# Performance work log

Measured on AMD Instinct MI355X. Metric: run time of the kernel, lower is better.

Reference implementation:

```python
import jax, jax.numpy as jnp
import numpy as np

L, N, EMB, H = 4, 50000, 128, 4
R, HID, LBL = 16, 64, 32
E = 625000


def setup_inputs() -> dict:
    key = jax.random.key(0)
    ks = jax.random.split(key, 10)
    s = 0.05
    return {
        "embedding": jax.random.normal(ks[0], (L, N, EMB), jnp.float32),
        "in_proj_w": jax.random.normal(ks[1], (3 * EMB, EMB), jnp.float32) * s,
        "in_proj_b": jnp.zeros((3 * EMB,), jnp.float32),
        "out_proj_w": jax.random.normal(ks[2], (EMB, EMB), jnp.float32) * s,
        "out_proj_b": jnp.zeros((EMB,), jnp.float32),
        "w1": jax.random.normal(ks[3], (R, EMB, HID), jnp.float32) * s,
        "root1": jax.random.normal(ks[4], (EMB, HID), jnp.float32) * s,
        "b1": jnp.zeros((HID,), jnp.float32),
        "w2": jax.random.normal(ks[5], (R, HID, LBL), jnp.float32) * s,
        "root2": jax.random.normal(ks[6], (HID, LBL), jnp.float32) * s,
        "b2": jnp.zeros((LBL,), jnp.float32),
        "edge_index": jax.random.randint(ks[7], (2, E), 0, N, dtype=jnp.int64),
        "edge_type": jax.random.randint(ks[8], (E,), 0, R, dtype=jnp.int64),
    }


def mha_self(x, wi, bi, wo, bo):
    # x: (L, N, EMB) -- torch nn.MultiheadAttention, batch_first=False, q=k=v=x
    Ls, Ns, Es = x.shape
    hd = Es // H
    qkv = x @ wi.T + bi                      # (L, N, 3E)
    q, k, v = jnp.split(qkv, 3, axis=-1)
    q = q.reshape(Ls, Ns, H, hd)
    k = k.reshape(Ls, Ns, H, hd)
    v = v.reshape(Ls, Ns, H, hd)
    scores = jnp.einsum('lnhd,mnhd->nhlm', q, k) / np.sqrt(hd).astype(np.float32)
    attn = jax.nn.softmax(scores, axis=-1)
    out = jnp.einsum('nhlm,mnhd->lnhd', attn, v).reshape(Ls, Ns, Es)
    return out @ wo.T + bo


def rgcn_layer(x, src, dst, etype, W, root, bias):
    # PyG RGCNConv (num_bases=None, aggr='mean'):
    # out[n] = x[n] @ root + bias + sum_r mean_{e: dst=n, type=r} x[src_e] @ W[r]
    Rr, fin, fout = W.shape
    seg = etype * N + dst                                   # (E,) combined (rel, dst)
    msg_sum = jax.ops.segment_sum(x[src], seg, num_segments=Rr * N)   # (R*N, fin)
    cnt = jax.ops.segment_sum(jnp.ones((src.shape[0],), x.dtype), seg,
                              num_segments=Rr * N)
    mean = (msg_sum / jnp.maximum(cnt, 1.0)[:, None]).reshape(Rr, N, fin)
    agg = jnp.einsum('rni,rio->no', mean, W)                # per-relation GEMM
    return agg + x @ root + bias


def reference(embedding, in_proj_w, in_proj_b, out_proj_w, out_proj_b,
              w1, root1, b1, w2, root2, b2, edge_index, edge_type):
    attn_out = mha_self(embedding, in_proj_w, in_proj_b, out_proj_w, out_proj_b)
    x = attn_out[0]                                         # (N, EMB)
    src, dst = edge_index[0], edge_index[1]
    x = jax.nn.relu(rgcn_layer(x, src, dst, edge_type, w1, root1, b1))
    x = rgcn_layer(x, src, dst, edge_type, w2, root2, b2)
    return jax.nn.softmax(x, axis=-1)
```

## Files before the change

kernel.cpp:

```cpp
#include <hip/hip_runtime.h>
#include <hip/hip_bf16.h>
#include <math.h>

#define NNODES 50000
#define NEDGE 625000
#define RREL 16
#define SCAN_NB 196

typedef __attribute__((ext_vector_type(8))) short short8;
typedef __attribute__((ext_vector_type(4))) float f32x4;

__device__ __forceinline__ float bfu(ushort u) {
  return __uint_as_float(((unsigned)u) << 16);
}
__device__ __forceinline__ ushort f2b(float f) {
  __hip_bfloat16 h = __float2bfloat16(f);
  return *(ushort*)&h;
}

__global__ __launch_bounds__(256) void prep_weights(
    const float* __restrict__ ipw, const float* __restrict__ opw,
    const float* __restrict__ w1, const float* __restrict__ root1,
    const float* __restrict__ w2, const float* __restrict__ root2,
    __hip_bfloat16* __restrict__ BTqkv, __hip_bfloat16* __restrict__ BToutT,
    __hip_bfloat16* __restrict__ BT1, __hip_bfloat16* __restrict__ BT2) {
  int i = blockIdx.x * 256 + threadIdx.x;
  if (i < 49152) {
    BTqkv[i] = __float2bfloat16(ipw[i]);
  } else if (i < 65536) {
    int j = i - 49152; int m = j / 128, c = j % 128;
    BToutT[j] = __float2bfloat16(opw[c * 128 + m]);
  } else if (i < 65536 + 139264) {
    int j = i - 65536; int c = j / 128, k = j % 128;
    float v;
    if (c < 64) v = root1[k * 64 + c];
    else { int r = (c - 64) >> 6, o = (c - 64) & 63; v = w1[r * 8192 + k * 64 + o]; }
    BT1[j] = __float2bfloat16(v);
  } else if (i < 65536 + 139264 + 34816) {
    int j = i - 65536 - 139264; int c = j / 64, k = j % 64;
    float v;
    if (c < 32) v = root2[k * 32 + c];
    else { int r = (c - 32) >> 5, o = (c - 32) & 31; v = w2[r * 2048 + k * 32 + o]; }
    BT2[j] = __float2bfloat16(v);
  }
}

__global__ __launch_bounds__(256) void prep_bias1(
    const float* __restrict__ opb, const float* __restrict__ w1,
    const float* __restrict__ root1, float* __restrict__ bias1) {
  int j = blockIdx.x * 256 + threadIdx.x;
  if (j >= 1088) return;
  float s = 0.f;
  if (j < 64) {
    for (int c = 0; c < 128; c++) s += opb[c] * root1[c * 64 + j];
  } else {
    int r = (j - 64) >> 6, o = (j - 64) & 63;
    for (int c = 0; c < 128; c++) s += opb[c] * w1[r * 8192 + c * 64 + o];
  }
  bias1[j] = s;
}

__global__ __launch_bounds__(256) void qkv_gemm(
    const float* __restrict__ A, const __hip_bfloat16* __restrict__ BT,
    const float* __restrict__ bias, __hip_bfloat16* __restrict__ C) {
  __shared__ ushort As[128 * 128];
  __shared__ ushort Cs[128 * 136];
  const int t = threadIdx.x;
  const long row0 = (long)blockIdx.x * 128;

#pragma unroll
  for (int c = t; c < 128 * 16; c += 256) {
    int r = c >> 4, cc = c & 15;
    long gm = row0 + r;
    int4 v = make_int4(0, 0, 0, 0);
    if (gm < 200000) {
      const float* ap = A + gm * 128 + cc * 8;
      float4 f0 = *(const float4*)ap;
      float4 f1 = *(const float4*)(ap + 4);
      v.x = (int)f2b(f0.x) | ((int)f2b(f0.y) << 16);
      v.y = (int)f2b(f0.z) | ((int)f2b(f0.w) << 16);
      v.z = (int)f2b(f1.x) | ((int)f2b(f1.y) << 16);
      v.w = (int)f2b(f1.z) | ((int)f2b(f1.w) << 16);
    }
    *(int4*)(As + r * 128 + ((cc ^ (r & 7)) * 8)) = v;
  }
  __syncthreads();

  const int lane = t & 63, w = t >> 6;
  const int wr = (w >> 1) * 64, wc = (w & 1) * 64;
  const int lrow = lane & 15, lk = lane >> 4;
  const int nstrips = (row0 < NNODES) ? 3 : 2;

  for (int s = 0; s < nstrips; s++) {
    const int col0 = (s == 2) ? 0 : 128 + s * 128;
    const long Meff = (s == 2) ? NNODES : 200000;

    const ushort* bp[4];
#pragma unroll
    for (int j = 0; j < 4; j++)
      bp[j] = (const ushort*)BT + (long)(col0 + wc + j * 16 + lrow) * 128 + lk * 8;

    f32x4 acc[4][4];
#pragma unroll
    for (int i = 0; i < 4; i++)
#pragma unroll
      for (int j = 0; j < 4; j++) acc[i][j] = (f32x4){0.f, 0.f, 0.f, 0.f};

#pragma unroll
    for (int k0 = 0; k0 < 128; k0 += 32) {
      const int cb = k0 / 8 + lk;
      short8 af[4], bfr[4];
#pragma unroll
      for (int j = 0; j < 4; j++) bfr[j] = *(const short8*)(bp[j] + k0);
#pragma unroll
      for (int i = 0; i < 4; i++) {
        int ra = wr + i * 16 + lrow;
        af[i] = *(const short8*)(As + ra * 128 + ((cb ^ (ra & 7)) * 8));
      }
#pragma unroll
      for (int i = 0; i < 4; i++)
#pragma unroll
        for (int j = 0; j < 4; j++)
          acc[i][j] = __builtin_amdgcn_mfma_f32_16x16x32_bf16(af[i], bfr[j], acc[i][j], 0, 0, 0);
    }

    __syncthreads();
#pragma unroll
    for (int j = 0; j < 4; j++) {
      int coll = wc + j * 16 + lrow;
      float bv = bias[col0 + coll];
#pragma unroll
      for (int i = 0; i < 4; i++) {
        int rbase = wr + i * 16 + lk * 4;
#pragma unroll
        for (int q = 0; q < 4; q++)
          Cs[(rbase + q) * 136 + coll] = f2b(acc[i][j][q] + bv);
      }
    }
    __syncthreads();
#pragma unroll
    for (int idx = t; idx < 128 * 16; idx += 256) {
      int r = idx >> 4, k = idx & 15;
      long gm = row0 + r;
      if (gm < Meff)
        *(int4*)((ushort*)C + gm * 384 + col0 + k * 8) = *(const int4*)(Cs + r * 136 + k * 8);
    }
  }
}

#define EPILOGUE_STORE(MEFF, NCOLS, LDC, BIASEXPR)                              \
  for (int p = 0; p < 2; p++) {                                                 \
    __syncthreads();                                                            \
    if ((w >> 1) == p) {                                                        \
      _Pragma("unroll")                                                         \
      for (int j = 0; j < 4; j++) {                                             \
        int coll = wc + j * 16 + lrow;                                          \
        float bv = (BIASEXPR);                                                  \
        _Pragma("unroll")                                                       \
        for (int i = 0; i < 4; i++) {                                           \
          int rloc = i * 16 + lk * 4;                                           \
          _Pragma("unroll")                                                     \
          for (int q = 0; q < 4; q++)                                           \
            Cs[(rloc + q) * 132 + coll] = f2b(acc[i][j][q] + bv);               \
        }                                                                       \
      }                                                                         \
    }                                                                           \
    __syncthreads();                                                            \
    _Pragma("unroll")                                                           \
    for (int idx = t; idx < 64 * 16; idx += 256) {                              \
      int r = idx >> 4, k = idx & 15;                                           \
      long gm = row0 + p * 64 + r;                                              \
      int col = col0 + k * 8;                                                   \
      if (gm < (MEFF) && col < (NCOLS))                                         \
        *(int4*)((ushort*)C + gm * (LDC) + col) = *(const int4*)(Cs + r * 132 + k * 8); \
    }                                                                           \
  }

template <int K>
__global__ __launch_bounds__(256) void gemm_strips(
    const __hip_bfloat16* __restrict__ Av, const __hip_bfloat16* __restrict__ BT,
    const float* __restrict__ bias, __hip_bfloat16* __restrict__ C,
    int M, int N, int ldc, int spg) {
  constexpr int CPR = K / 8;
  __shared__ ushort As[128 * K];
  __shared__ ushort Cs[64 * 132];
  const int t = threadIdx.x;
  const long row0 = (long)blockIdx.x * 128;

#pragma unroll
  for (int c = t; c < 128 * CPR; c += 256) {
    int r = c / CPR, cc = c % CPR;
    long gm = row0 + r;
    int4 v = make_int4(0, 0, 0, 0);
    if (gm < M) v = *(const int4*)((const ushort*)Av + gm * K + cc * 8);
    *(int4*)(As + r * K + ((cc ^ (r & 7)) * 8)) = v;
  }
  __syncthreads();

  const int lane = t & 63, w = t >> 6;
  const int wr = (w >> 1) * 64, wc = (w & 1) * 64;
  const int lrow = lane & 15, lk = lane >> 4;
  const int nstrips = (N + 127) / 128;
  const int sbeg = blockIdx.y * spg;
  const int send = min(sbeg + spg, nstrips);

  for (int s = sbeg; s < send; s++) {
    const int col0 = s * 128;

    const ushort* bp[4];
#pragma unroll
    for (int j = 0; j < 4; j++) {
      int gn = col0 + wc + j * 16 + lrow;
      if (gn > N - 1) gn = N - 1;
      bp[j] = (const ushort*)BT + (long)gn * K + lk * 8;
    }

    f32x4 acc[4][4];
#pragma unroll
    for (int i = 0; i < 4; i++)
#pragma unroll
      for (int j = 0; j < 4; j++) acc[i][j] = (f32x4){0.f, 0.f, 0.f, 0.f};

#pragma unroll
    for (int k0 = 0; k0 < K; k0 += 32) {
      const int cb = k0 / 8 + lk;
      short8 af[4], bfr[4];
#pragma unroll
      for (int j = 0; j < 4; j++) bfr[j] = *(const short8*)(bp[j] + k0);
#pragma unroll
      for (int i = 0; i < 4; i++) {
        int ra = wr + i * 16 + lrow;
        af[i] = *(const short8*)(As + ra * K + ((cb ^ (ra & 7)) * 8));
      }
#pragma unroll
      for (int i = 0; i < 4; i++)
#pragma unroll
        for (int j = 0; j < 4; j++)
          acc[i][j] = __builtin_amdgcn_mfma_f32_16x16x32_bf16(af[i], bfr[j], acc[i][j], 0, 0, 0);
    }

    EPILOGUE_STORE(M, N, ldc, bias ? bias[min(col0 + coll, N - 1)] : 0.f)
  }
}

__global__ __launch_bounds__(256) void attn_kernel(
    const __hip_bfloat16* __restrict__ qkv, __hip_bfloat16* __restrict__ o0) {
  int w = threadIdx.x >> 6, lane = threadIdx.x & 63;
  int n = blockIdx.x * 4 + w;
  const ushort* base = (const ushort*)qkv;
  uint qv = *(const uint*)(base + (size_t)n * 384 + lane * 2);
  float q0 = bfu(qv & 0xffff), q1 = bfu(qv >> 16);
  float s[4];
#pragma unroll
  for (int m = 0; m < 4; m++) {
    uint kk = *(const uint*)(base + (size_t)(m * NNODES + n) * 384 + 128 + lane * 2);
    float p = q0 * bfu(kk & 0xffff) + q1 * bfu(kk >> 16);
#pragma unroll
    for (int off = 8; off; off >>= 1) p += __shfl_xor(p, off);
    s[m] = p * 0.17677669529663687f;
  }
  float mx = fmaxf(fmaxf(s[0], s[1]), fmaxf(s[2], s[3]));
  float e[4], sum = 0.f;
#pragma unroll
  for (int m = 0; m < 4; m++) { e[m] = __expf(s[m] - mx); sum += e[m]; }
  float inv = 1.0f / sum;
  float o0f = 0.f, o1f = 0.f;
#pragma unroll
  for (int m = 0; m < 4; m++) {
    uint vv = *(const uint*)(base + (size_t)(m * NNODES + n) * 384 + 256 + lane * 2);
    float wgt = e[m] * inv;
    o0f += wgt * bfu(vv & 0xffff);
    o1f += wgt * bfu(vv >> 16);
  }
  *(uint*)((ushort*)o0 + (size_t)n * 128 + lane * 2) = (uint)f2b(o0f) | ((uint)f2b(o1f) << 16);
}

__global__ __launch_bounds__(256) void count_edges(
    const int* __restrict__ dst, const int* __restrict__ et, int* __restrict__ cnt) {
  int e = blockIdx.x * 256 + threadIdx.x;
  if (e < NEDGE) atomicAdd(&cnt[et[e] * NNODES + dst[e]], 1);
}

__global__ __launch_bounds__(256) void scan1(
    const int* __restrict__ cnt, int* __restrict__ off, int* __restrict__ part) {
  int t = threadIdx.x, b = blockIdx.x;
  int i = b * 256 + t;
  int v = 0;
  if (i < NNODES) {
#pragma unroll
    for (int r = 0; r < RREL; r++) v += cnt[r * NNODES + i];
  }
  __shared__ int sm[256];
  sm[t] = v;
  __syncthreads();
#pragma unroll
  for (int o = 1; o < 256; o <<= 1) {
    int x = (t >= o) ? sm[t - o] : 0;
    __syncthreads();
    sm[t] += x;
    __syncthreads();
  }
  if (i < NNODES) off[i] = sm[t] - v;
  if (t == 255) part[b] = sm[t];
}

__global__ __launch_bounds__(256) void scan2(int* __restrict__ part) {
  int t = threadIdx.x;
  int v = (t < SCAN_NB) ? part[t] : 0;
  __shared__ int sm[256];
  sm[t] = v;
  __syncthreads();
#pragma unroll
  for (int o = 1; o < 256; o <<= 1) {
    int x = (t >= o) ? sm[t - o] : 0;
    __syncthreads();
    sm[t] += x;
    __syncthreads();
  }
  if (t < SCAN_NB) part[t] = sm[t] - v;
}

__global__ __launch_bounds__(256) void scan3(int* __restrict__ off, const int* __restrict__ part) {
  int i = blockIdx.x * 256 + threadIdx.x;
  if (i < NNODES) off[i] += part[blockIdx.x];
  if (i == 0) off[NNODES] = NEDGE;
}

__global__ __launch_bounds__(256) void scatter_edges(
    const int* __restrict__ src, const int* __restrict__ dst, const int* __restrict__ et,
    const int* __restrict__ cnt, const int* __restrict__ off,
    int* __restrict__ fill, unsigned* __restrict__ sorted, float* __restrict__ scales) {
  int e = blockIdx.x * 256 + threadIdx.x;
  if (e >= NEDGE) return;
  int d = dst[e], r = et[e], s = src[e];
  int pos = off[d] + atomicAdd(&fill[d], 1);
  sorted[pos] = (unsigned)s | ((unsigned)r << 16);
  scales[pos] = 1.0f / (float)cnt[r * NNODES + d];
}

__global__ __launch_bounds__(256) void fused1(
    const int* __restrict__ off, const unsigned* __restrict__ sorted,
    const float* __restrict__ scales, const ushort* __restrict__ Y1,
    const float* __restrict__ b1, __hip_bfloat16* __restrict__ x1b) {
  int w = threadIdx.x >> 6, lane = threadIdx.x & 63;
  int d = blockIdx.x * 4 + w;
  int s0 = off[d], s1 = off[d + 1];
  float a0 = bfu(Y1[(size_t)d * 1088 + lane]) + b1[lane];
  float a1 = 0.f, a2 = 0.f, a3 = 0.f;
  int i = s0;
  for (; i + 3 < s1; i += 4) {
    unsigned p0 = sorted[i], p1 = sorted[i + 1], p2 = sorted[i + 2], p3 = sorted[i + 3];
    float c0 = scales[i], c1 = scales[i + 1], c2 = scales[i + 2], c3 = scales[i + 3];
    a0 += bfu(Y1[(size_t)(p0 & 0xFFFF) * 1088 + 64 + (p0 >> 16) * 64 + lane]) * c0;
    a1 += bfu(Y1[(size_t)(p1 & 0xFFFF) * 1088 + 64 + (p1 >> 16) * 64 + lane]) * c1;
    a2 += bfu(Y1[(size_t)(p2 & 0xFFFF) * 1088 + 64 + (p2 >> 16) * 64 + lane]) * c2;
    a3 += bfu(Y1[(size_t)(p3 & 0xFFFF) * 1088 + 64 + (p3 >> 16) * 64 + lane]) * c3;
  }
  for (; i < s1; i++) {
    unsigned p = sorted[i];
    a0 += bfu(Y1[(size_t)(p & 0xFFFF) * 1088 + 64 + (p >> 16) * 64 + lane]) * scales[i];
  }
  float acc = (a0 + a1) + (a2 + a3);
  x1b[(size_t)d * 64 + lane] = __float2bfloat16(fmaxf(acc, 0.f));
}

__global__ __launch_bounds__(256) void fused2(
    const int* __restrict__ off, const unsigned* __restrict__ sorted,
    const float* __restrict__ scales, const ushort* __restrict__ Y2,
    const float* __restrict__ b2, float* __restrict__ out) {
  int w = threadIdx.x >> 6, lane = threadIdx.x & 63;
  int d = blockIdx.x * 4 + w;
  int j = lane & 31, half = lane >> 5;
  int s0 = off[d], s1 = off[d + 1];
  float a0 = 0.f, a1 = 0.f;
  int i = s0 + half;
  for (; i + 2 < s1; i += 4) {
    unsigned p0 = sorted[i], p1 = sorted[i + 2];
    a0 += bfu(Y2[(size_t)(p0 & 0xFFFF) * 544 + 32 + (p0 >> 16) * 32 + j]) * scales[i];
    a1 += bfu(Y2[(size_t)(p1 & 0xFFFF) * 544 + 32 + (p1 >> 16) * 32 + j]) * scales[i + 2];
  }
  for (; i < s1; i += 2) {
    unsigned p = sorted[i];
    a0 += bfu(Y2[(size_t)(p & 0xFFFF) * 544 + 32 + (p >> 16) * 32 + j]) * scales[i];
  }
  float acc = a0 + a1;
  acc += __shfl_xor(acc, 32);
  float v = acc + bfu(Y2[(size_t)d * 544 + j]) + b2[j];
  float mx = v;
#pragma unroll
  for (int o = 16; o; o >>= 1) mx = fmaxf(mx, __shfl_xor(mx, o));
  float e = __expf(v - mx);
  float sum = e;
#pragma unroll
  for (int o = 16; o; o >>= 1) sum += __shfl_xor(sum, o);
  if (half == 0) out[(size_t)d * 32 + j] = e / sum;
}

extern "C" void kernel_launch(void* const* d_in, const int* in_sizes, int n_in,
                              void* d_out, int out_size, void* d_ws, size_t ws_size,
                              hipStream_t stream) {
  (void)in_sizes; (void)n_in; (void)out_size; (void)ws_size;
  const float* emb   = (const float*)d_in[0];
  const float* ipw   = (const float*)d_in[1];
  const float* ipb   = (const float*)d_in[2];
  const float* opw   = (const float*)d_in[3];
  const float* opb   = (const float*)d_in[4];
  const float* w1    = (const float*)d_in[5];
  const float* root1 = (const float*)d_in[6];
  const float* b1    = (const float*)d_in[7];
  const float* w2    = (const float*)d_in[8];
  const float* root2 = (const float*)d_in[9];
  const float* b2    = (const float*)d_in[10];
  const int*   eidx  = (const int*)d_in[11];
  const int*   etype = (const int*)d_in[12];
  const int* srcp = eidx;
  const int* dstp = eidx + NEDGE;

  unsigned char* ws = (unsigned char*)d_ws;
  size_t off_b = 0;
  auto alloc = [&](size_t bytes) {
    unsigned char* p = ws + off_b;
    off_b += (bytes + 255) & ~(size_t)255;
    return p;
  };

  unsigned char* R = alloc(153600000);
  __hip_bfloat16* qkv = (__hip_bfloat16*)R;
  __hip_bfloat16* Y1  = (__hip_bfloat16*)R;
  __hip_bfloat16* Y2  = (__hip_bfloat16*)R;
  __hip_bfloat16* o0  = (__hip_bfloat16*)alloc(12800000);
  __hip_bfloat16* x1b = (__hip_bfloat16*)alloc(6400000);
  int*            cnt = (int*)alloc(3200000);
  int*            offs = (int*)alloc((NNODES + 1) * 4);
  int*            fill = (int*)alloc(NNODES * 4);
  int*            part = (int*)alloc(SCAN_NB * 4);
  unsigned*       sorted = (unsigned*)alloc(NEDGE * 4);
  float*          scales = (float*)alloc(NEDGE * 4);
  __hip_bfloat16* BTqkv  = (__hip_bfloat16*)alloc(98304);
  __hip_bfloat16* BToutT = (__hip_bfloat16*)alloc(32768);
  __hip_bfloat16* BT1    = (__hip_bfloat16*)alloc(278528);
  __hip_bfloat16* BT2    = (__hip_bfloat16*)alloc(69632);
  __hip_bfloat16* BW     = (__hip_bfloat16*)alloc(278528);
  float*          bias1  = (float*)alloc(4352);

  prep_weights<<<dim3((241664 + 255) / 256), dim3(256), 0, stream>>>(
      ipw, opw, w1, root1, w2, root2, BTqkv, BToutT, BT1, BT2);
  prep_bias1<<<dim3(5), dim3(256), 0, stream>>>(opb, w1, root1, bias1);
  hipMemsetAsync(cnt, 0, (size_t)RREL * NNODES * sizeof(int), stream);
  hipMemsetAsync(fill, 0, (size_t)NNODES * sizeof(int), stream);
  count_edges<<<dim3((NEDGE + 255) / 256), dim3(256), 0, stream>>>(dstp, etype, cnt);
  scan1<<<dim3(SCAN_NB), dim3(256), 0, stream>>>(cnt, offs, part);
  scan2<<<dim3(1), dim3(256), 0, stream>>>(part);
  scan3<<<dim3(SCAN_NB), dim3(256), 0, stream>>>(offs, part);
  scatter_edges<<<dim3((NEDGE + 255) / 256), dim3(256), 0, stream>>>(
      srcp, dstp, etype, cnt, offs, fill, sorted, scales);

  gemm_strips<128><<<dim3(9, 1), dim3(256), 0, stream>>>(
      BT1, BToutT, nullptr, BW, 1088, 128, 128, 1);

  qkv_gemm<<<dim3(1563), dim3(256), 0, stream>>>(emb, BTqkv, ipb, qkv);

  attn_kernel<<<dim3(12500), dim3(256), 0, stream>>>(qkv, o0);

  gemm_strips<128><<<dim3(391, 3), dim3(256), 0, stream>>>(
      o0, BW, bias1, Y1, NNODES, 1088, 1088, 3);

  fused1<<<dim3(NNODES / 4), dim3(256), 0, stream>>>(
      offs, sorted, scales, (const ushort*)Y1, b1, x1b);

  gemm_strips<64><<<dim3(391, 2), dim3(256), 0, stream>>>(
      x1b, BT2, nullptr, Y2, NNODES, 544, 544, 3);

  fused2<<<dim3(NNODES / 4), dim3(256), 0, stream>>>(
      offs, sorted, scales, (const ushort*)Y2, b2, (float*)d_out);
}
```

Baseline: 340.2 us.

## Fuse QKV projection and per-node attention into one kernel

Replaces the separate QKV GEMM and attention kernels with a single kernel. Each block handles 32 nodes across all 4 sequence positions, computes Q (position 0 only, pre-scaled), K and V with MFMA into shared memory, then runs the softmax-attention in place. This removes the 150MB bf16 qkv round trip through global memory and one launch. In exchange, the B-matrix fragments are re-read from global per block, and the tiles are smaller, which may lower MFMA efficiency.

```diff
diff --git a/kernel.cpp b/kernel.cpp
--- a/kernel.cpp
+++ b/kernel.cpp
@@ -60,91 +60,138 @@
   bias1[j] = s;
 }
 
-__global__ __launch_bounds__(256) void qkv_gemm(
-    const float* __restrict__ A, const __hip_bfloat16* __restrict__ BT,
-    const float* __restrict__ bias, __hip_bfloat16* __restrict__ C) {
-  __shared__ ushort As[128 * 128];
-  __shared__ ushort Cs[128 * 136];
+__global__ __launch_bounds__(256) void attn_mega(
+    const float* __restrict__ emb, const __hip_bfloat16* __restrict__ BTqkv,
+    const float* __restrict__ ipb, __hip_bfloat16* __restrict__ o0) {
+  __shared__ ushort Ks[128 * 132];
+  __shared__ ushort Vs[128 * 132];
+  __shared__ ushort Qs[32 * 132];
+  const ushort* BT = (const ushort*)BTqkv;
   const int t = threadIdx.x;
-  const long row0 = (long)blockIdx.x * 128;
-
-#pragma unroll
-  for (int c = t; c < 128 * 16; c += 256) {
-    int r = c >> 4, cc = c & 15;
-    long gm = row0 + r;
-    int4 v = make_int4(0, 0, 0, 0);
-    if (gm < 200000) {
-      const float* ap = A + gm * 128 + cc * 8;
-      float4 f0 = *(const float4*)ap;
-      float4 f1 = *(const float4*)(ap + 4);
+  const int w = t >> 6, lane = t & 63;
+  const int lrow = lane & 15, lk = lane >> 4;
+  const long nb = (long)blockIdx.x * 32;
+
+  short8 af[2][4];
+#pragma unroll
+  for (int i = 0; i < 2; i++) {
+    long n = nb + 16 * i + lrow;
+    if (n > NNODES - 1) n = NNODES - 1;
+    const float* ap = emb + ((long)w * NNODES + n) * 128;
+#pragma unroll
+    for (int k0 = 0; k0 < 4; k0++) {
+      float4 f0 = *(const float4*)(ap + k0 * 32 + lk * 8);
+      float4 f1 = *(const float4*)(ap + k0 * 32 + lk * 8 + 4);
+      int4 v;
       v.x = (int)f2b(f0.x) | ((int)f2b(f0.y) << 16);
       v.y = (int)f2b(f0.z) | ((int)f2b(f0.w) << 16);
       v.z = (int)f2b(f1.x) | ((int)f2b(f1.y) << 16);
       v.w = (int)f2b(f1.z) | ((int)f2b(f1.w) << 16);
-    }
-    *(int4*)(As + r * 128 + ((cc ^ (r & 7)) * 8)) = v;
+      af[i][k0] = *(short8*)&v;
+    }
+  }
+
+  const float alpha = 0.17677669529663687f;
+
+  if (w == 0) {
+#pragma unroll
+    for (int half = 0; half < 2; half++) {
+      f32x4 acc[2][4];
+#pragma unroll
+      for (int i = 0; i < 2; i++)
+#pragma unroll
+        for (int j = 0; j < 4; j++) acc[i][j] = (f32x4){0.f, 0.f, 0.f, 0.f};
+#pragma unroll
+      for (int k0 = 0; k0 < 4; k0++) {
+        short8 bfr[4];
+#pragma unroll
+        for (int j = 0; j < 4; j++)
+          bfr[j] = *(const short8*)(BT + (long)(half * 64 + j * 16 + lrow) * 128 + k0 * 32 + lk * 8);
+#pragma unroll
+        for (int i = 0; i < 2; i++)
+#pragma unroll
+          for (int j = 0; j < 4; j++)
+            acc[i][j] = __builtin_amdgcn_mfma_f32_16x16x32_bf16(af[i][k0], bfr[j], acc[i][j], 0, 0, 0);
+      }
+#pragma unroll
+      for (int j = 0; j < 4; j++) {
+        int c = half * 64 + j * 16 + lrow;
+        float bq = ipb[c];
+#pragma unroll
+        for (int i = 0; i < 2; i++)
+#pragma unroll
+          for (int q = 0; q < 4; q++)
+            Qs[(16 * i + 4 * lk + q) * 132 + c] = f2b((acc[i][j][q] + bq) * alpha);
+      }
+    }
+  }
+
+#pragma unroll
+  for (int sidx = 0; sidx < 2; sidx++) {
+    const int base = 128 + sidx * 128;
+    ushort* dst = sidx ? Vs : Ks;
+#pragma unroll
+    for (int half = 0; half < 2; half++) {
+      f32x4 acc[2][4];
+#pragma unroll
+      for (int i = 0; i < 2; i++)
+#pragma unroll
+        for (int j = 0; j < 4; j++) acc[i][j] = (f32x4){0.f, 0.f, 0.f, 0.f};
+#pragma unroll
+      for (int k0 = 0; k0 < 4; k0++) {
+        short8 bfr[4];
+#pragma unroll
+        for (int j = 0; j < 4; j++)
+          bfr[j] = *(const short8*)(BT + (long)(base + half * 64 + j * 16 + lrow) * 128 + k0 * 32 + lk * 8);
+#pragma unroll
+        for (int i = 0; i < 2; i++)
+#pragma unroll
+          for (int j = 0; j < 4; j++)
+            acc[i][j] = __builtin_amdgcn_mfma_f32_16x16x32_bf16(af[i][k0], bfr[j], acc[i][j], 0, 0, 0);
+      }
+#pragma unroll
+      for (int j = 0; j < 4; j++) {
+        int c = half * 64 + j * 16 + lrow;
+        float bv = ipb[base + c];
+#pragma unroll
+        for (int i = 0; i < 2; i++)
+#pragma unroll
+          for (int q = 0; q < 4; q++)
+            dst[(32 * w + 16 * i + 4 * lk + q) * 132 + c] = f2b(acc[i][j][q] + bv);
+      }
+    }
   }
   __syncthreads();
 
-  const int lane = t & 63, w = t >> 6;
-  const int wr = (w >> 1) * 64, wc = (w & 1) * 64;
-  const int lrow = lane & 15, lk = lane >> 4;
-  const int nstrips = (row0 < NNODES) ? 3 : 2;
-
-  for (int s = 0; s < nstrips; s++) {
-    const int col0 = (s == 2) ? 0 : 128 + s * 128;
-    const long Meff = (s == 2) ? NNODES : 200000;
-
-    const ushort* bp[4];
-#pragma unroll
-    for (int j = 0; j < 4; j++)
-      bp[j] = (const ushort*)BT + (long)(col0 + wc + j * 16 + lrow) * 128 + lk * 8;
-
-    f32x4 acc[4][4];
-#pragma unroll
-    for (int i = 0; i < 4; i++)
-#pragma unroll
-      for (int j = 0; j < 4; j++) acc[i][j] = (f32x4){0.f, 0.f, 0.f, 0.f};
-
-#pragma unroll
-    for (int k0 = 0; k0 < 128; k0 += 32) {
-      const int cb = k0 / 8 + lk;
-      short8 af[4], bfr[4];
-#pragma unroll
-      for (int j = 0; j < 4; j++) bfr[j] = *(const short8*)(bp[j] + k0);
-#pragma unroll
-      for (int i = 0; i < 4; i++) {
-        int ra = wr + i * 16 + lrow;
-        af[i] = *(const short8*)(As + ra * 128 + ((cb ^ (ra & 7)) * 8));
-      }
-#pragma unroll
-      for (int i = 0; i < 4; i++)
-#pragma unroll
-        for (int j = 0; j < 4; j++)
-          acc[i][j] = __builtin_amdgcn_mfma_f32_16x16x32_bf16(af[i], bfr[j], acc[i][j], 0, 0, 0);
-    }
-
-    __syncthreads();
-#pragma unroll
-    for (int j = 0; j < 4; j++) {
-      int coll = wc + j * 16 + lrow;
-      float bv = bias[col0 + coll];
-#pragma unroll
-      for (int i = 0; i < 4; i++) {
-        int rbase = wr + i * 16 + lk * 4;
-#pragma unroll
-        for (int q = 0; q < 4; q++)
-          Cs[(rbase + q) * 136 + coll] = f2b(acc[i][j][q] + bv);
-      }
-    }
-    __syncthreads();
-#pragma unroll
-    for (int idx = t; idx < 128 * 16; idx += 256) {
-      int r = idx >> 4, k = idx & 15;
-      long gm = row0 + r;
-      if (gm < Meff)
-        *(int4*)((ushort*)C + gm * 384 + col0 + k * 8) = *(const int4*)(Cs + r * 136 + k * 8);
-    }
+  for (int ii = 0; ii < 8; ii++) {
+    int i = 8 * w + ii;
+    long n = nb + i;
+    uint qv = *(const uint*)(Qs + i * 132 + lane * 2);
+    float q0 = bfu(qv & 0xffff), q1 = bfu(qv >> 16);
+    float s[4];
+#pragma unroll
+    for (int m = 0; m < 4; m++) {
+      uint kk = *(const uint*)(Ks + (m * 32 + i) * 132 + lane * 2);
+      float p = q0 * bfu(kk & 0xffff) + q1 * bfu(kk >> 16);
+#pragma unroll
+      for (int off = 8; off; off >>= 1) p += __shfl_xor(p, off);
+      s[m] = p;
+    }
+    float mx = fmaxf(fmaxf(s[0], s[1]), fmaxf(s[2], s[3]));
+    float e[4], sum = 0.f;
+#pragma unroll
+    for (int m = 0; m < 4; m++) { e[m] = __expf(s[m] - mx); sum += e[m]; }
+    float inv = 1.0f / sum;
+    float o0f = 0.f, o1f = 0.f;
+#pragma unroll
+    for (int m = 0; m < 4; m++) {
+      uint vv = *(const uint*)(Vs + (m * 32 + i) * 132 + lane * 2);
+      float wgt = e[m] * inv;
+      o0f += wgt * bfu(vv & 0xffff);
+      o1f += wgt * bfu(vv >> 16);
+    }
+    if (n < NNODES)
+      *(uint*)((ushort*)o0 + n * 128 + lane * 2) = (uint)f2b(o0f) | ((uint)f2b(o1f) << 16);
   }
 }
 
@@ -243,38 +290,6 @@
   }
 }
 
-__global__ __launch_bounds__(256) void attn_kernel(
-    const __hip_bfloat16* __restrict__ qkv, __hip_bfloat16* __restrict__ o0) {
-  int w = threadIdx.x >> 6, lane = threadIdx.x & 63;
-  int n = blockIdx.x * 4 + w;
-  const ushort* base = (const ushort*)qkv;
-  uint qv = *(const uint*)(base + (size_t)n * 384 + lane * 2);
-  float q0 = bfu(qv & 0xffff), q1 = bfu(qv >> 16);
-  float s[4];
-#pragma unroll
-  for (int m = 0; m < 4; m++) {
-    uint kk = *(const uint*)(base + (size_t)(m * NNODES + n) * 384 + 128 + lane * 2);
-    float p = q0 * bfu(kk & 0xffff) + q1 * bfu(kk >> 16);
-#pragma unroll
-    for (int off = 8; off; off >>= 1) p += __shfl_xor(p, off);
-    s[m] = p * 0.17677669529663687f;
-  }
-  float mx = fmaxf(fmaxf(s[0], s[1]), fmaxf(s[2], s[3]));
-  float e[4], sum = 0.f;
-#pragma unroll
-  for (int m = 0; m < 4; m++) { e[m] = __expf(s[m] - mx); sum += e[m]; }
-  float inv = 1.0f / sum;
-  float o0f = 0.f, o1f = 0.f;
-#pragma unroll
-  for (int m = 0; m < 4; m++) {
-    uint vv = *(const uint*)(base + (size_t)(m * NNODES + n) * 384 + 256 + lane * 2);
-    float wgt = e[m] * inv;
-    o0f += wgt * bfu(vv & 0xffff);
-    o1f += wgt * bfu(vv >> 16);
-  }
-  *(uint*)((ushort*)o0 + (size_t)n * 128 + lane * 2) = (uint)f2b(o0f) | ((uint)f2b(o1f) << 16);
-}
-
 __global__ __launch_bounds__(256) void count_edges(
     const int* __restrict__ dst, const int* __restrict__ et, int* __restrict__ cnt) {
   int e = blockIdx.x * 256 + threadIdx.x;
@@ -424,8 +439,7 @@
     return p;
   };
 
-  unsigned char* R = alloc(153600000);
-  __hip_bfloat16* qkv = (__hip_bfloat16*)R;
+  unsigned char* R = alloc(108800000);
   __hip_bfloat16* Y1  = (__hip_bfloat16*)R;
   __hip_bfloat16* Y2  = (__hip_bfloat16*)R;
   __hip_bfloat16* o0  = (__hip_bfloat16*)alloc(12800000);
@@ -458,9 +472,8 @@
   gemm_strips<128><<<dim3(9, 1), dim3(256), 0, stream>>>(
       BT1, BToutT, nullptr, BW, 1088, 128, 128, 1);
 
-  qkv_gemm<<<dim3(1563), dim3(256), 0, stream>>>(emb, BTqkv, ipb, qkv);
-
-  attn_kernel<<<dim3(12500), dim3(256), 0, stream>>>(qkv, o0);
+  attn_mega<<<dim3((NNODES + 31) / 32), dim3(256), 0, stream>>>(
+      emb, BTqkv, ipb, o0);
 
   gemm_strips<128><<<dim3(391, 3), dim3(256), 0, stream>>>(
       o0, BW, bias1, Y1, NNODES, 1088, 1088, 3);
```

Measured after the change: 339.0 us. About the same (-0.4%).
